# Optimization experiments

Measured on AMD Instinct MI355X. Metric: run time of the kernel, lower is better.

Reference implementation:

```python
import jax, jax.numpy as jnp
import numpy as np

WS = 8          # window_size
NH = 4          # num_heads
C = 128         # embed_dim
HD = C // NH    # head_dim
HID = 4 * C     # mlp hidden
EPS = 1e-5


def _rel_pos_index(ws):
    coords = np.stack(np.meshgrid(np.arange(ws), np.arange(ws), indexing='ij')).reshape(2, -1)
    rel = coords[:, :, None] - coords[:, None, :]          # (2, N, N)
    rel = rel.transpose(1, 2, 0).astype(np.int64)          # (N, N, 2)
    rel[..., 0] += ws - 1
    rel[..., 1] += ws - 1
    rel[..., 0] *= 2 * ws - 1
    return rel.sum(-1)                                     # (N, N)


def _layernorm(x, g, b):
    mu = jnp.mean(x, axis=-1, keepdims=True)
    var = jnp.mean(jnp.square(x - mu), axis=-1, keepdims=True)
    return (x - mu) * jax.lax.rsqrt(var + EPS) * g + b


def setup_inputs() -> dict:
    key = jax.random.key(0)
    ks = jax.random.split(key, 12)
    B, L = 32, 4096
    s = 0.02
    return {
        'x': jax.random.normal(ks[0], (B, L, C), jnp.float32),
        'W_qkv': jax.random.normal(ks[1], (C, 3 * C), jnp.float32) * s,
        'b_qkv': jnp.zeros((3 * C,), jnp.float32),
        'W_out': jax.random.normal(ks[2], (C, C), jnp.float32) * s,
        'b_out': jnp.zeros((C,), jnp.float32),
        'bias_table': jax.random.normal(ks[3], ((2 * WS - 1) ** 2, NH), jnp.float32) * s,
        'g1': jnp.ones((C,), jnp.float32), 'be1': jnp.zeros((C,), jnp.float32),
        'g2': jnp.ones((C,), jnp.float32), 'be2': jnp.zeros((C,), jnp.float32),
        'W_fc1': jax.random.normal(ks[4], (C, HID), jnp.float32) * s,
        'b_fc1': jnp.zeros((HID,), jnp.float32),
        'W_fc2': jax.random.normal(ks[5], (HID, C), jnp.float32) * s,
        'b_fc2': jnp.zeros((C,), jnp.float32),
        'H': 64, 'W': 64,
    }


def reference(x, W_qkv, b_qkv, W_out, b_out, bias_table, g1, be1, g2, be2,
              W_fc1, b_fc1, W_fc2, b_fc2, H, W):
    B, L, _ = x.shape
    N = WS * WS
    shortcut = x
    xn = _layernorm(x, g1, be1)
    # window partition: (B,H,W,C) -> (B*nw, N, C)
    xw = xn.reshape(B, H // WS, WS, W // WS, WS, C)
    xw = xw.transpose(0, 1, 3, 2, 4, 5).reshape(-1, N, C)
    # attention
    qkv = (xw @ W_qkv + b_qkv).reshape(-1, N, 3, NH, HD)
    q, k, v = jnp.moveaxis(qkv, 2, 0)                      # each (Bw, N, NH, HD)
    attn = jnp.einsum('bnhd,bmhd->bhnm', q, k) * (HD ** -0.5)
    idx = jnp.asarray(_rel_pos_index(WS))                  # (N, N)
    bias = bias_table[idx].transpose(2, 0, 1)              # (NH, N, N)
    attn = jax.nn.softmax((attn + bias[None]).astype(jnp.float32), axis=-1).astype(x.dtype)
    o = jnp.einsum('bhnm,bmhd->bnhd', attn, v).reshape(-1, N, C)
    o = o @ W_out + b_out
    # window reverse
    o = o.reshape(B, H // WS, W // WS, WS, WS, C)
    o = o.transpose(0, 1, 3, 2, 4, 5).reshape(B, L, C)
    x = shortcut + o
    # MLP block
    xn = _layernorm(x, g2, be2)
    h = jax.nn.gelu(xn @ W_fc1 + b_fc1, approximate=False)
    return x + (h @ W_fc2 + b_fc2)
```

## Files before the change

kernel.cpp:

```cpp
#include <hip/hip_runtime.h>
#include <hip/hip_bf16.h>

typedef __bf16 bf16;
typedef __bf16 bf16x8 __attribute__((ext_vector_type(8)));
typedef float f32x4 __attribute__((ext_vector_type(4)));

#define C_DIM 128
#define LDA 136
#define LDQ 40
#define LDVT 72
#define LDP 72
#define LDH 264

__device__ __forceinline__ f32x4 mfma16(bf16x8 a, bf16x8 b, f32x4 c) {
  return __builtin_amdgcn_mfma_f32_16x16x32_bf16(a, b, c, 0, 0, 0);
}


__global__ __launch_bounds__(256, 2) void swin_fused(
    const float* __restrict__ x,
    const bf16*  __restrict__ Wqkv_t, const float* __restrict__ b_qkv,
    const bf16*  __restrict__ Wout_t, const float* __restrict__ b_out,
    const float* __restrict__ btabx,
    const float* __restrict__ g1, const float* __restrict__ be1,
    const float* __restrict__ g2, const float* __restrict__ be2,
    const bf16*  __restrict__ Wfc1_t, const float* __restrict__ b_fc1,
    const bf16*  __restrict__ Wfc2_t, const float* __restrict__ b_fc2,
    float* __restrict__ out)
{
  __shared__ __attribute__((aligned(16))) char smem[76800];
  bf16 (*sA)[LDA]       = (bf16(*)[LDA])(smem);
  bf16 (*sQ)[64][LDQ]   = (bf16(*)[64][LDQ])(smem + 17408);
  bf16 (*sK)[64][LDQ]   = (bf16(*)[64][LDQ])(smem + 37888);
  bf16 (*sVT)[32][LDVT] = (bf16(*)[32][LDVT])(smem + 58368);
  bf16 (*sP)[64][LDP]   = (bf16(*)[64][LDP])(smem + 17408);
  bf16 (*sY)[LDA]       = (bf16(*)[LDA])(smem + 17408);
  bf16 (*sH)[LDH]       = (bf16(*)[LDH])(smem + 17408);

  const int tid = threadIdx.x;
  const int w   = tid >> 6;
  const int l   = tid & 63;
  const int l15 = l & 15;
  const int lhi = l >> 4;

  const int win = blockIdx.x;
  const int b   = win >> 6;
  const int wy  = (win >> 3) & 7;
  const int wx  = win & 7;
  const int rowbase = b * 4096 + wy * 512 + wx * 8;

  float yreg[2][4][4];

  {
    const int tok = tid >> 2, seg = tid & 3;
    const int t = rowbase + (tok >> 3) * 64 + (tok & 7);
    const float* xr = x + (size_t)t * C_DIM + seg * 32;
    float f[32]; float s = 0.f, s2 = 0.f;
    #pragma unroll
    for (int i = 0; i < 8; i++) {
      f32x4 v = *(const f32x4*)(xr + i * 4);
      #pragma unroll
      for (int j = 0; j < 4; j++) { float a = v[j]; f[i*4+j] = a; s += a; s2 += a*a; }
    }
    s  += __shfl_xor(s, 1);  s  += __shfl_xor(s, 2);
    s2 += __shfl_xor(s2, 1); s2 += __shfl_xor(s2, 2);
    float mu = s * (1.f/128.f);
    float rs = rsqrtf(s2 * (1.f/128.f) - mu*mu + 1e-5f);
    #pragma unroll
    for (int i = 0; i < 4; i++) {
      f32x4 gv0 = *(const f32x4*)(g1  + seg*32 + i*8);
      f32x4 gv1 = *(const f32x4*)(g1  + seg*32 + i*8 + 4);
      f32x4 bv0 = *(const f32x4*)(be1 + seg*32 + i*8);
      f32x4 bv1 = *(const f32x4*)(be1 + seg*32 + i*8 + 4);
      bf16x8 o;
      #pragma unroll
      for (int j = 0; j < 4; j++) {
        o[j]   = (bf16)((f[i*8+j]   - mu) * rs * gv0[j] + bv0[j]);
        o[j+4] = (bf16)((f[i*8+j+4] - mu) * rs * gv1[j] + bv1[j]);
      }
      *(bf16x8*)&sA[tok][seg*32 + i*8] = o;
    }
  }
  __syncthreads();

  {
    bf16x8 a[4][4];
    #pragma unroll
    for (int mt = 0; mt < 4; mt++)
      #pragma unroll
      for (int ks = 0; ks < 4; ks++)
        a[mt][ks] = *(const bf16x8*)&sA[mt*16 + l15][ks*32 + lhi*8];
    const float scale = 0.17677669529663687f;
    #pragma unroll
    for (int nti = 0; nti < 6; nti++) {
      const int nt = w * 6 + nti;
      const int colg = nt * 16 + l15;
      const bf16* wp = Wqkv_t + (size_t)colg * 128 + lhi * 8;
      bf16x8 bw[4];
      #pragma unroll
      for (int ks = 0; ks < 4; ks++) bw[ks] = *(const bf16x8*)(wp + ks * 32);
      const float bias = b_qkv[colg];
      const int kind = colg >> 7;
      const int h    = (colg >> 5) & 3;
      const int d    = colg & 31;
      #pragma unroll
      for (int mt = 0; mt < 4; mt++) {
        f32x4 acc = {0.f, 0.f, 0.f, 0.f};
        #pragma unroll
        for (int ks = 0; ks < 4; ks++) acc = mfma16(a[mt][ks], bw[ks], acc);
        #pragma unroll
        for (int r = 0; r < 4; r++) {
          const int token = mt*16 + lhi*4 + r;
          float v = acc[r] + bias;
          if (kind == 0)      sQ[h][token][d] = (bf16)(v * scale);
          else if (kind == 1) sK[h][token][d] = (bf16)v;
          else                sVT[h][d][token] = (bf16)v;
        }
      }
    }
  }
  __syncthreads();

  {
    const int h = w;
    bf16x8 aq[4], bk[4];
    #pragma unroll
    for (int mt = 0; mt < 4; mt++) aq[mt] = *(const bf16x8*)&sQ[h][mt*16 + l15][lhi*8];
    #pragma unroll
    for (int ct = 0; ct < 4; ct++) bk[ct] = *(const bf16x8*)&sK[h][ct*16 + l15][lhi*8];
    f32x4 sc[4][4];
    #pragma unroll
    for (int mt = 0; mt < 4; mt++)
      #pragma unroll
      for (int ct = 0; ct < 4; ct++) {
        f32x4 z = {0.f, 0.f, 0.f, 0.f};
        sc[mt][ct] = mfma16(aq[mt], bk[ct], z);
      }
    __syncthreads();
    #pragma unroll
    for (int mt = 0; mt < 4; mt++) {
      #pragma unroll
      for (int r = 0; r < 4; r++) {
        const int n = mt*16 + lhi*4 + r;
        f32x4 bv = *(const f32x4*)(btabx + (((h*64 + n)*16 + l15) << 2));
        float rv[4];
        #pragma unroll
        for (int ct = 0; ct < 4; ct++) rv[ct] = sc[mt][ct][r] + bv[ct];
        float mx = fmaxf(fmaxf(rv[0], rv[1]), fmaxf(rv[2], rv[3]));
        #pragma unroll
        for (int o = 1; o < 16; o <<= 1) mx = fmaxf(mx, __shfl_xor(mx, o));
        float sum = 0.f;
        #pragma unroll
        for (int ct = 0; ct < 4; ct++) { rv[ct] = __expf(rv[ct] - mx); sum += rv[ct]; }
        #pragma unroll
        for (int o = 1; o < 16; o <<= 1) sum += __shfl_xor(sum, o);
        const float inv = 1.f / sum;
        #pragma unroll
        for (int ct = 0; ct < 4; ct++) sP[h][n][ct*16 + l15] = (bf16)(rv[ct] * inv);
      }
    }
    f32x4 o_[4][2];
    #pragma unroll
    for (int mt = 0; mt < 4; mt++) { f32x4 z = {0.f,0.f,0.f,0.f}; o_[mt][0] = z; o_[mt][1] = z; }
    #pragma unroll
    for (int ks = 0; ks < 2; ks++) {
      bf16x8 ap[4], bvv[2];
      #pragma unroll
      for (int mt = 0; mt < 4; mt++) ap[mt] = *(const bf16x8*)&sP[h][mt*16 + l15][ks*32 + lhi*8];
      #pragma unroll
      for (int c2 = 0; c2 < 2; c2++) bvv[c2] = *(const bf16x8*)&sVT[h][c2*16 + l15][ks*32 + lhi*8];
      #pragma unroll
      for (int mt = 0; mt < 4; mt++)
        #pragma unroll
        for (int c2 = 0; c2 < 2; c2++) o_[mt][c2] = mfma16(ap[mt], bvv[c2], o_[mt][c2]);
    }
    #pragma unroll
    for (int mt = 0; mt < 4; mt++)
      #pragma unroll
      for (int c2 = 0; c2 < 2; c2++)
        #pragma unroll
        for (int r = 0; r < 4; r++)
          sA[mt*16 + lhi*4 + r][h*32 + c2*16 + l15] = (bf16)o_[mt][c2][r];
  }
  __syncthreads();

  {
    bf16x8 a[4][4];
    #pragma unroll
    for (int mt = 0; mt < 4; mt++)
      #pragma unroll
      for (int ks = 0; ks < 4; ks++)
        a[mt][ks] = *(const bf16x8*)&sA[mt*16 + l15][ks*32 + lhi*8];
    #pragma unroll
    for (int nto = 0; nto < 2; nto++) {
      const int col = (w*2 + nto) * 16 + l15;
      const bf16* wp = Wout_t + (size_t)col * 128 + lhi * 8;
      bf16x8 bw[4];
      #pragma unroll
      for (int ks = 0; ks < 4; ks++) bw[ks] = *(const bf16x8*)(wp + ks * 32);
      const float bo = b_out[col];
      #pragma unroll
      for (int mt = 0; mt < 4; mt++) {
        f32x4 acc = {0.f, 0.f, 0.f, 0.f};
        #pragma unroll
        for (int ks = 0; ks < 4; ks++) acc = mfma16(a[mt][ks], bw[ks], acc);
        #pragma unroll
        for (int r = 0; r < 4; r++) {
          const int token = mt*16 + lhi*4 + r;
          const int t = rowbase + (token >> 3) * 64 + (token & 7);
          float v = acc[r] + bo + x[(size_t)t * C_DIM + col];
          yreg[nto][mt][r] = v;
          sY[token][col] = (bf16)v;
        }
      }
    }
  }
  __syncthreads();

  {
    const int tok = tid >> 2, seg = tid & 3;
    float f[32]; float s = 0.f, s2 = 0.f;
    #pragma unroll
    for (int i = 0; i < 4; i++) {
      bf16x8 v = *(const bf16x8*)&sY[tok][seg*32 + i*8];
      #pragma unroll
      for (int j = 0; j < 8; j++) { float a = (float)v[j]; f[i*8+j] = a; s += a; s2 += a*a; }
    }
    s  += __shfl_xor(s, 1);  s  += __shfl_xor(s, 2);
    s2 += __shfl_xor(s2, 1); s2 += __shfl_xor(s2, 2);
    float mu = s * (1.f/128.f);
    float rs = rsqrtf(s2 * (1.f/128.f) - mu*mu + 1e-5f);
    #pragma unroll
    for (int i = 0; i < 4; i++) {
      f32x4 gv0 = *(const f32x4*)(g2  + seg*32 + i*8);
      f32x4 gv1 = *(const f32x4*)(g2  + seg*32 + i*8 + 4);
      f32x4 bv0 = *(const f32x4*)(be2 + seg*32 + i*8);
      f32x4 bv1 = *(const f32x4*)(be2 + seg*32 + i*8 + 4);
      bf16x8 o;
      #pragma unroll
      for (int j = 0; j < 4; j++) {
        o[j]   = (bf16)((f[i*8+j]   - mu) * rs * gv0[j] + bv0[j]);
        o[j+4] = (bf16)((f[i*8+j+4] - mu) * rs * gv1[j] + bv1[j]);
      }
      *(bf16x8*)&sA[tok][seg*32 + i*8] = o;
    }
  }
  __syncthreads();

  {
    bf16x8 a[4][4];
    #pragma unroll
    for (int mt = 0; mt < 4; mt++)
      #pragma unroll
      for (int ks = 0; ks < 4; ks++)
        a[mt][ks] = *(const bf16x8*)&sA[mt*16 + l15][ks*32 + lhi*8];
    f32x4 accF[2][4];
    #pragma unroll
    for (int i = 0; i < 2; i++)
      #pragma unroll
      for (int mt = 0; mt < 4; mt++) { f32x4 z = {0.f,0.f,0.f,0.f}; accF[i][mt] = z; }

    #pragma unroll
    for (int hf = 0; hf < 2; hf++) {
      #pragma unroll
      for (int nti = 0; nti < 4; nti++) {
        const int ntg    = hf*16 + w*4 + nti;
        const int colh   = ntg*16 + l15;
        const int colloc = (w*4 + nti)*16 + l15;
        const bf16* wp = Wfc1_t + (size_t)colh * 128 + lhi * 8;
        bf16x8 bw[4];
        #pragma unroll
        for (int ks = 0; ks < 4; ks++) bw[ks] = *(const bf16x8*)(wp + ks * 32);
        const float bb = b_fc1[colh];
        #pragma unroll
        for (int mt = 0; mt < 4; mt++) {
          f32x4 acc = {0.f, 0.f, 0.f, 0.f};
          #pragma unroll
          for (int ks = 0; ks < 4; ks++) acc = mfma16(a[mt][ks], bw[ks], acc);
          #pragma unroll
          for (int r = 0; r < 4; r++) {
            float v = acc[r] + bb;
            float u = v * (0.7978845608028654f + 0.0356774081363001f * v * v);
            float e = __expf(2.f * u);
            float th = 1.f - 2.f / (e + 1.f);
            float g = 0.5f * v * (1.f + th);
            sH[mt*16 + lhi*4 + r][colloc] = (bf16)g;
          }
        }
      }
      __syncthreads();
      #pragma unroll
      for (int ks = 0; ks < 8; ks++) {
        bf16x8 ah[4], bw2[2];
        #pragma unroll
        for (int mt = 0; mt < 4; mt++) ah[mt] = *(const bf16x8*)&sH[mt*16 + l15][ks*32 + lhi*8];
        #pragma unroll
        for (int nto = 0; nto < 2; nto++)
          bw2[nto] = *(const bf16x8*)(Wfc2_t + (size_t)((w*2 + nto)*16 + l15) * 512 + hf*256 + ks*32 + lhi*8);
        #pragma unroll
        for (int nto = 0; nto < 2; nto++)
          #pragma unroll
          for (int mt = 0; mt < 4; mt++) accF[nto][mt] = mfma16(ah[mt], bw2[nto], accF[nto][mt]);
      }
      __syncthreads();
    }
    #pragma unroll
    for (int nto = 0; nto < 2; nto++) {
      const int col = (w*2 + nto)*16 + l15;
      const float bb = b_fc2[col];
      #pragma unroll
      for (int mt = 0; mt < 4; mt++)
        #pragma unroll
        for (int r = 0; r < 4; r++) {
          const int token = mt*16 + lhi*4 + r;
          const int t = rowbase + (token >> 3) * 64 + (token & 7);
          out[(size_t)t * C_DIM + col] = accF[nto][mt][r] + bb + yreg[nto][mt][r];
        }
    }
  }
}

__global__ void prep_transpose(
    const float* __restrict__ Wqkv, const float* __restrict__ Wout,
    const float* __restrict__ Wfc1, const float* __restrict__ Wfc2,
    const float* __restrict__ btab,
    bf16* __restrict__ Wqkv_t, bf16* __restrict__ Wout_t,
    bf16* __restrict__ Wfc1_t, bf16* __restrict__ Wfc2_t,
    float* __restrict__ btabx)
{
  int i = blockIdx.x * 256 + threadIdx.x;
  if (i < 49152) { int n = i >> 7, k = i & 127; Wqkv_t[i] = (bf16)Wqkv[k*384 + n]; return; }
  i -= 49152;
  if (i < 16384) { int n = i >> 7, k = i & 127; Wout_t[i] = (bf16)Wout[k*128 + n]; return; }
  i -= 16384;
  if (i < 65536) { int n = i >> 7, k = i & 127; Wfc1_t[i] = (bf16)Wfc1[k*512 + n]; return; }
  i -= 65536;
  if (i < 65536) { int n = i >> 9, k = i & 511; Wfc2_t[i] = (bf16)Wfc2[k*128 + n]; return; }
  i -= 65536;
  if (i < 16384) {
    int ct  = i & 3;
    int l15 = (i >> 2) & 15;
    int n   = (i >> 6) & 63;
    int h   = i >> 12;
    int m = ct * 16 + l15;
    int nr = n >> 3, nc = n & 7, mr = m >> 3, mc = m & 7;
    int idx = (nr - mr + 7) * 15 + (nc - mc + 7);
    btabx[i] = btab[idx * 4 + h];
  }
}

extern "C" void kernel_launch(void* const* d_in, const int* in_sizes, int n_in,
                              void* d_out, int out_size, void* d_ws, size_t ws_size,
                              hipStream_t stream)
{
  const float* x    = (const float*)d_in[0];
  const float* Wqkv = (const float*)d_in[1];
  const float* bqkv = (const float*)d_in[2];
  const float* Wout = (const float*)d_in[3];
  const float* bout = (const float*)d_in[4];
  const float* btab = (const float*)d_in[5];
  const float* g1   = (const float*)d_in[6];
  const float* be1  = (const float*)d_in[7];
  const float* g2   = (const float*)d_in[8];
  const float* be2  = (const float*)d_in[9];
  const float* Wfc1 = (const float*)d_in[10];
  const float* bfc1 = (const float*)d_in[11];
  const float* Wfc2 = (const float*)d_in[12];
  const float* bfc2 = (const float*)d_in[13];

  bf16* ws = (bf16*)d_ws;
  bf16* Wqkv_t = ws;
  bf16* Wout_t = ws + 49152;
  bf16* Wfc1_t = ws + 65536;
  bf16* Wfc2_t = ws + 131072;
  float* btabx = (float*)(ws + 196608);

  prep_transpose<<<832, 256, 0, stream>>>(Wqkv, Wout, Wfc1, Wfc2, btab,
                                          Wqkv_t, Wout_t, Wfc1_t, Wfc2_t, btabx);

  const int B = in_sizes[0] / (4096 * 128);
  swin_fused<<<dim3(B * 64), 256, 0, stream>>>(
      x, Wqkv_t, bqkv, Wout_t, bout, btabx, g1, be1, g2, be2,
      Wfc1_t, bfc1, Wfc2_t, bfc2, (float*)d_out);
}
```

Before: 195.0 us.

## Double block to 512 threads and halve per-wave work across all stages

Launches 8 waves per window instead of 4. Each stage is split more finely: LayerNorm uses 8 lanes per token, QKV uses 3 tiles per wave, attention gives each head's 64 query rows to two waves, and the out-proj/FC1/FC2 stages use one 16-column tile per wave. The fp32 residual registers are dropped; the residual is kept as bf16 in shared memory (sY moved to the sVT region) and re-read for the final add, which lowers residual precision. The new launch bounds of (512,4) cap registers much more tightly, so spills are possible, and LDS use of about 75KB per block still limits how many blocks fit on a CU.

```diff
diff --git a/kernel.cpp b/kernel.cpp
--- a/kernel.cpp
+++ b/kernel.cpp
@@ -17,7 +17,7 @@
 }
 
 
-__global__ __launch_bounds__(256, 2) void swin_fused(
+__global__ __launch_bounds__(512, 4) void swin_fused(
     const float* __restrict__ x,
     const bf16*  __restrict__ Wqkv_t, const float* __restrict__ b_qkv,
     const bf16*  __restrict__ Wout_t, const float* __restrict__ b_out,
@@ -32,10 +32,10 @@
   bf16 (*sA)[LDA]       = (bf16(*)[LDA])(smem);
   bf16 (*sQ)[64][LDQ]   = (bf16(*)[64][LDQ])(smem + 17408);
   bf16 (*sK)[64][LDQ]   = (bf16(*)[64][LDQ])(smem + 37888);
+  bf16 (*sP)[64][LDP]   = (bf16(*)[64][LDP])(smem + 17408);
+  bf16 (*sH)[LDH]       = (bf16(*)[LDH])(smem + 17408);
   bf16 (*sVT)[32][LDVT] = (bf16(*)[32][LDVT])(smem + 58368);
-  bf16 (*sP)[64][LDP]   = (bf16(*)[64][LDP])(smem + 17408);
-  bf16 (*sY)[LDA]       = (bf16(*)[LDA])(smem + 17408);
-  bf16 (*sH)[LDH]       = (bf16(*)[LDH])(smem + 17408);
+  bf16 (*sY)[LDA]       = (bf16(*)[LDA])(smem + 58368);
 
   const int tid = threadIdx.x;
   const int w   = tid >> 6;
@@ -49,36 +49,34 @@
   const int wx  = win & 7;
   const int rowbase = b * 4096 + wy * 512 + wx * 8;
 
-  float yreg[2][4][4];
-
-  {
-    const int tok = tid >> 2, seg = tid & 3;
+  {
+    const int tok = tid >> 3, seg = tid & 7;
     const int t = rowbase + (tok >> 3) * 64 + (tok & 7);
-    const float* xr = x + (size_t)t * C_DIM + seg * 32;
-    float f[32]; float s = 0.f, s2 = 0.f;
-    #pragma unroll
-    for (int i = 0; i < 8; i++) {
+    const float* xr = x + (size_t)t * C_DIM + seg * 16;
+    float f[16]; float s = 0.f, s2 = 0.f;
+    #pragma unroll
+    for (int i = 0; i < 4; i++) {
       f32x4 v = *(const f32x4*)(xr + i * 4);
       #pragma unroll
       for (int j = 0; j < 4; j++) { float a = v[j]; f[i*4+j] = a; s += a; s2 += a*a; }
     }
-    s  += __shfl_xor(s, 1);  s  += __shfl_xor(s, 2);
-    s2 += __shfl_xor(s2, 1); s2 += __shfl_xor(s2, 2);
+    s  += __shfl_xor(s, 1);  s  += __shfl_xor(s, 2);  s  += __shfl_xor(s, 4);
+    s2 += __shfl_xor(s2, 1); s2 += __shfl_xor(s2, 2); s2 += __shfl_xor(s2, 4);
     float mu = s * (1.f/128.f);
     float rs = rsqrtf(s2 * (1.f/128.f) - mu*mu + 1e-5f);
     #pragma unroll
-    for (int i = 0; i < 4; i++) {
-      f32x4 gv0 = *(const f32x4*)(g1  + seg*32 + i*8);
-      f32x4 gv1 = *(const f32x4*)(g1  + seg*32 + i*8 + 4);
-      f32x4 bv0 = *(const f32x4*)(be1 + seg*32 + i*8);
-      f32x4 bv1 = *(const f32x4*)(be1 + seg*32 + i*8 + 4);
+    for (int i = 0; i < 2; i++) {
+      f32x4 gv0 = *(const f32x4*)(g1  + seg*16 + i*8);
+      f32x4 gv1 = *(const f32x4*)(g1  + seg*16 + i*8 + 4);
+      f32x4 bv0 = *(const f32x4*)(be1 + seg*16 + i*8);
+      f32x4 bv1 = *(const f32x4*)(be1 + seg*16 + i*8 + 4);
       bf16x8 o;
       #pragma unroll
       for (int j = 0; j < 4; j++) {
         o[j]   = (bf16)((f[i*8+j]   - mu) * rs * gv0[j] + bv0[j]);
         o[j+4] = (bf16)((f[i*8+j+4] - mu) * rs * gv1[j] + bv1[j]);
       }
-      *(bf16x8*)&sA[tok][seg*32 + i*8] = o;
+      *(bf16x8*)&sA[tok][seg*16 + i*8] = o;
     }
   }
   __syncthreads();
@@ -92,8 +90,8 @@
         a[mt][ks] = *(const bf16x8*)&sA[mt*16 + l15][ks*32 + lhi*8];
     const float scale = 0.17677669529663687f;
     #pragma unroll
-    for (int nti = 0; nti < 6; nti++) {
-      const int nt = w * 6 + nti;
+    for (int nti = 0; nti < 3; nti++) {
+      const int nt = w * 3 + nti;
       const int colg = nt * 16 + l15;
       const bf16* wp = Wqkv_t + (size_t)colg * 128 + lhi * 8;
       bf16x8 bw[4];
@@ -122,30 +120,32 @@
   __syncthreads();
 
   {
-    const int h = w;
-    bf16x8 aq[4], bk[4];
-    #pragma unroll
-    for (int mt = 0; mt < 4; mt++) aq[mt] = *(const bf16x8*)&sQ[h][mt*16 + l15][lhi*8];
+    const int h    = w >> 1;
+    const int half = w & 1;
+    bf16x8 aq[2], bk[4];
+    #pragma unroll
+    for (int mtl = 0; mtl < 2; mtl++)
+      aq[mtl] = *(const bf16x8*)&sQ[h][(half*2 + mtl)*16 + l15][lhi*8];
     #pragma unroll
     for (int ct = 0; ct < 4; ct++) bk[ct] = *(const bf16x8*)&sK[h][ct*16 + l15][lhi*8];
-    f32x4 sc[4][4];
-    #pragma unroll
-    for (int mt = 0; mt < 4; mt++)
+    f32x4 sc[2][4];
+    #pragma unroll
+    for (int mtl = 0; mtl < 2; mtl++)
       #pragma unroll
       for (int ct = 0; ct < 4; ct++) {
         f32x4 z = {0.f, 0.f, 0.f, 0.f};
-        sc[mt][ct] = mfma16(aq[mt], bk[ct], z);
+        sc[mtl][ct] = mfma16(aq[mtl], bk[ct], z);
       }
     __syncthreads();
     #pragma unroll
-    for (int mt = 0; mt < 4; mt++) {
+    for (int mtl = 0; mtl < 2; mtl++) {
       #pragma unroll
       for (int r = 0; r < 4; r++) {
-        const int n = mt*16 + lhi*4 + r;
+        const int n = (half*2 + mtl)*16 + lhi*4 + r;
         f32x4 bv = *(const f32x4*)(btabx + (((h*64 + n)*16 + l15) << 2));
         float rv[4];
         #pragma unroll
-        for (int ct = 0; ct < 4; ct++) rv[ct] = sc[mt][ct][r] + bv[ct];
+        for (int ct = 0; ct < 4; ct++) rv[ct] = sc[mtl][ct][r] + bv[ct];
         float mx = fmaxf(fmaxf(rv[0], rv[1]), fmaxf(rv[2], rv[3]));
         #pragma unroll
         for (int o = 1; o < 16; o <<= 1) mx = fmaxf(mx, __shfl_xor(mx, o));
@@ -159,28 +159,30 @@
         for (int ct = 0; ct < 4; ct++) sP[h][n][ct*16 + l15] = (bf16)(rv[ct] * inv);
       }
     }
-    f32x4 o_[4][2];
-    #pragma unroll
-    for (int mt = 0; mt < 4; mt++) { f32x4 z = {0.f,0.f,0.f,0.f}; o_[mt][0] = z; o_[mt][1] = z; }
+    f32x4 o_[2][2];
+    #pragma unroll
+    for (int mtl = 0; mtl < 2; mtl++) { f32x4 z = {0.f,0.f,0.f,0.f}; o_[mtl][0] = z; o_[mtl][1] = z; }
     #pragma unroll
     for (int ks = 0; ks < 2; ks++) {
-      bf16x8 ap[4], bvv[2];
-      #pragma unroll
-      for (int mt = 0; mt < 4; mt++) ap[mt] = *(const bf16x8*)&sP[h][mt*16 + l15][ks*32 + lhi*8];
-      #pragma unroll
-      for (int c2 = 0; c2 < 2; c2++) bvv[c2] = *(const bf16x8*)&sVT[h][c2*16 + l15][ks*32 + lhi*8];
-      #pragma unroll
-      for (int mt = 0; mt < 4; mt++)
-        #pragma unroll
-        for (int c2 = 0; c2 < 2; c2++) o_[mt][c2] = mfma16(ap[mt], bvv[c2], o_[mt][c2]);
-    }
-    #pragma unroll
-    for (int mt = 0; mt < 4; mt++)
+      bf16x8 ap[2], bvv[2];
+      #pragma unroll
+      for (int mtl = 0; mtl < 2; mtl++)
+        ap[mtl] = *(const bf16x8*)&sP[h][(half*2 + mtl)*16 + l15][ks*32 + lhi*8];
       #pragma unroll
       for (int c2 = 0; c2 < 2; c2++)
+        bvv[c2] = *(const bf16x8*)&sVT[h][c2*16 + l15][ks*32 + lhi*8];
+      #pragma unroll
+      for (int mtl = 0; mtl < 2; mtl++)
+        #pragma unroll
+        for (int c2 = 0; c2 < 2; c2++) o_[mtl][c2] = mfma16(ap[mtl], bvv[c2], o_[mtl][c2]);
+    }
+    #pragma unroll
+    for (int mtl = 0; mtl < 2; mtl++)
+      #pragma unroll
+      for (int c2 = 0; c2 < 2; c2++)
         #pragma unroll
         for (int r = 0; r < 4; r++)
-          sA[mt*16 + lhi*4 + r][h*32 + c2*16 + l15] = (bf16)o_[mt][c2][r];
+          sA[(half*2 + mtl)*16 + lhi*4 + r][h*32 + c2*16 + l15] = (bf16)o_[mtl][c2][r];
   }
   __syncthreads();
 
@@ -191,58 +193,54 @@
       #pragma unroll
       for (int ks = 0; ks < 4; ks++)
         a[mt][ks] = *(const bf16x8*)&sA[mt*16 + l15][ks*32 + lhi*8];
-    #pragma unroll
-    for (int nto = 0; nto < 2; nto++) {
-      const int col = (w*2 + nto) * 16 + l15;
-      const bf16* wp = Wout_t + (size_t)col * 128 + lhi * 8;
-      bf16x8 bw[4];
-      #pragma unroll
-      for (int ks = 0; ks < 4; ks++) bw[ks] = *(const bf16x8*)(wp + ks * 32);
-      const float bo = b_out[col];
-      #pragma unroll
-      for (int mt = 0; mt < 4; mt++) {
-        f32x4 acc = {0.f, 0.f, 0.f, 0.f};
-        #pragma unroll
-        for (int ks = 0; ks < 4; ks++) acc = mfma16(a[mt][ks], bw[ks], acc);
-        #pragma unroll
-        for (int r = 0; r < 4; r++) {
-          const int token = mt*16 + lhi*4 + r;
-          const int t = rowbase + (token >> 3) * 64 + (token & 7);
-          float v = acc[r] + bo + x[(size_t)t * C_DIM + col];
-          yreg[nto][mt][r] = v;
-          sY[token][col] = (bf16)v;
-        }
-      }
-    }
-  }
-  __syncthreads();
-
-  {
-    const int tok = tid >> 2, seg = tid & 3;
-    float f[32]; float s = 0.f, s2 = 0.f;
-    #pragma unroll
-    for (int i = 0; i < 4; i++) {
-      bf16x8 v = *(const bf16x8*)&sY[tok][seg*32 + i*8];
+    const int col = w * 16 + l15;
+    const bf16* wp = Wout_t + (size_t)col * 128 + lhi * 8;
+    bf16x8 bw[4];
+    #pragma unroll
+    for (int ks = 0; ks < 4; ks++) bw[ks] = *(const bf16x8*)(wp + ks * 32);
+    const float bo = b_out[col];
+    #pragma unroll
+    for (int mt = 0; mt < 4; mt++) {
+      f32x4 acc = {0.f, 0.f, 0.f, 0.f};
+      #pragma unroll
+      for (int ks = 0; ks < 4; ks++) acc = mfma16(a[mt][ks], bw[ks], acc);
+      #pragma unroll
+      for (int r = 0; r < 4; r++) {
+        const int token = mt*16 + lhi*4 + r;
+        const int t = rowbase + (token >> 3) * 64 + (token & 7);
+        float v = acc[r] + bo + x[(size_t)t * C_DIM + col];
+        sY[token][col] = (bf16)v;
+      }
+    }
+  }
+  __syncthreads();
+
+  {
+    const int tok = tid >> 3, seg = tid & 7;
+    float f[16]; float s = 0.f, s2 = 0.f;
+    #pragma unroll
+    for (int i = 0; i < 2; i++) {
+      bf16x8 v = *(const bf16x8*)&sY[tok][seg*16 + i*8];
       #pragma unroll
       for (int j = 0; j < 8; j++) { float a = (float)v[j]; f[i*8+j] = a; s += a; s2 += a*a; }
     }
-    s  += __shfl_xor(s, 1);  s  += __shfl_xor(s, 2);
-    s2 += __shfl_xor(s2, 1); s2 += __shfl_xor(s2, 2);
+    s  += __shfl_xor(s, 1);  s  += __shfl_xor(s, 2);  s  += __shfl_xor(s, 4);
+    s2 += __shfl_xor(s2, 1); s2 += __shfl_xor(s2, 2); s2 += __shfl_xor(s2, 4);
     float mu = s * (1.f/128.f);
     float rs = rsqrtf(s2 * (1.f/128.f) - mu*mu + 1e-5f);
     #pragma unroll
-    for (int i = 0; i < 4; i++) {
-      f32x4 gv0 = *(const f32x4*)(g2  + seg*32 + i*8);
-      f32x4 gv1 = *(const f32x4*)(g2  + seg*32 + i*8 + 4);
-      f32x4 bv0 = *(const f32x4*)(be2 + seg*32 + i*8);
-      f32x4 bv1 = *(const f32x4*)(be2 + seg*32 + i*8 + 4);
+    for (int i = 0; i < 2; i++) {
+      f32x4 gv0 = *(const f32x4*)(g2  + seg*16 + i*8);
+      f32x4 gv1 = *(const f32x4*)(g2  + seg*16 + i*8 + 4);
+      f32x4 bv0 = *(const f32x4*)(be2 + seg*16 + i*8);
+      f32x4 bv1 = *(const f32x4*)(be2 + seg*16 + i*8 + 4);
       bf16x8 o;
       #pragma unroll
       for (int j = 0; j < 4; j++) {
         o[j]   = (bf16)((f[i*8+j]   - mu) * rs * gv0[j] + bv0[j]);
         o[j+4] = (bf16)((f[i*8+j+4] - mu) * rs * gv1[j] + bv1[j]);
       }
-      *(bf16x8*)&sA[tok][seg*32 + i*8] = o;
+      *(bf16x8*)&sA[tok][seg*16 + i*8] = o;
     }
   }
   __syncthreads();
@@ -254,19 +252,17 @@
       #pragma unroll
       for (int ks = 0; ks < 4; ks++)
         a[mt][ks] = *(const bf16x8*)&sA[mt*16 + l15][ks*32 + lhi*8];
-    f32x4 accF[2][4];
-    #pragma unroll
-    for (int i = 0; i < 2; i++)
-      #pragma unroll
-      for (int mt = 0; mt < 4; mt++) { f32x4 z = {0.f,0.f,0.f,0.f}; accF[i][mt] = z; }
+    f32x4 accF[4];
+    #pragma unroll
+    for (int mt = 0; mt < 4; mt++) { f32x4 z = {0.f,0.f,0.f,0.f}; accF[mt] = z; }
 
     #pragma unroll
     for (int hf = 0; hf < 2; hf++) {
       #pragma unroll
-      for (int nti = 0; nti < 4; nti++) {
-        const int ntg    = hf*16 + w*4 + nti;
+      for (int nti = 0; nti < 2; nti++) {
+        const int ntg    = hf*16 + w*2 + nti;
         const int colh   = ntg*16 + l15;
-        const int colloc = (w*4 + nti)*16 + l15;
+        const int colloc = (w*2 + nti)*16 + l15;
         const bf16* wp = Wfc1_t + (size_t)colh * 128 + lhi * 8;
         bf16x8 bw[4];
         #pragma unroll
@@ -291,32 +287,25 @@
       __syncthreads();
       #pragma unroll
       for (int ks = 0; ks < 8; ks++) {
-        bf16x8 ah[4], bw2[2];
+        bf16x8 ah[4];
         #pragma unroll
         for (int mt = 0; mt < 4; mt++) ah[mt] = *(const bf16x8*)&sH[mt*16 + l15][ks*32 + lhi*8];
-        #pragma unroll
-        for (int nto = 0; nto < 2; nto++)
-          bw2[nto] = *(const bf16x8*)(Wfc2_t + (size_t)((w*2 + nto)*16 + l15) * 512 + hf*256 + ks*32 + lhi*8);
-        #pragma unroll
-        for (int nto = 0; nto < 2; nto++)
-          #pragma unroll
-          for (int mt = 0; mt < 4; mt++) accF[nto][mt] = mfma16(ah[mt], bw2[nto], accF[nto][mt]);
+        bf16x8 bw2 = *(const bf16x8*)(Wfc2_t + (size_t)(w*16 + l15) * 512 + hf*256 + ks*32 + lhi*8);
+        #pragma unroll
+        for (int mt = 0; mt < 4; mt++) accF[mt] = mfma16(ah[mt], bw2, accF[mt]);
       }
       __syncthreads();
     }
-    #pragma unroll
-    for (int nto = 0; nto < 2; nto++) {
-      const int col = (w*2 + nto)*16 + l15;
-      const float bb = b_fc2[col];
-      #pragma unroll
-      for (int mt = 0; mt < 4; mt++)
-        #pragma unroll
-        for (int r = 0; r < 4; r++) {
-          const int token = mt*16 + lhi*4 + r;
-          const int t = rowbase + (token >> 3) * 64 + (token & 7);
-          out[(size_t)t * C_DIM + col] = accF[nto][mt][r] + bb + yreg[nto][mt][r];
-        }
-    }
+    const int col = w*16 + l15;
+    const float bb = b_fc2[col];
+    #pragma unroll
+    for (int mt = 0; mt < 4; mt++)
+      #pragma unroll
+      for (int r = 0; r < 4; r++) {
+        const int token = mt*16 + lhi*4 + r;
+        const int t = rowbase + (token >> 3) * 64 + (token & 7);
+        out[(size_t)t * C_DIM + col] = accF[mt][r] + bb + (float)sY[token][col];
+      }
   }
 }
 
@@ -379,7 +368,7 @@
                                           Wqkv_t, Wout_t, Wfc1_t, Wfc2_t, btabx);
 
   const int B = in_sizes[0] / (4096 * 128);
-  swin_fused<<<dim3(B * 64), 256, 0, stream>>>(
+  swin_fused<<<dim3(B * 64), 512, 0, stream>>>(
       x, Wqkv_t, bqkv, Wout_t, bout, btabx, g1, be1, g2, be2,
       Wfc1_t, bfc1, Wfc2_t, bfc2, (float*)d_out);
 }
```

New measurement: 194.6 us. No clear change (-0.2%).

## Software-prefetch weight tiles and residual inputs into registers ahead of MFMA use

Applied to the files above, without the earlier changes.

Adds register double-buffering for the global weight loads in the QKV, output-projection, FC1 and FC2 GEMMs. Each next weight tile is issued before the current MFMAs run, and the W_out weights and residual x values are loaded during the softmax phase. The goal is to hide global memory latency behind compute in each stage. It raises register pressure under launch_bounds(256,2), which could cause spills or lower occupancy.

```diff
diff --git a/kernel.cpp b/kernel.cpp
--- a/kernel.cpp
+++ b/kernel.cpp
@@ -91,15 +91,25 @@
       for (int ks = 0; ks < 4; ks++)
         a[mt][ks] = *(const bf16x8*)&sA[mt*16 + l15][ks*32 + lhi*8];
     const float scale = 0.17677669529663687f;
+    bf16x8 bw[4]; float bias;
+    {
+      const int colg0 = (w*6)*16 + l15;
+      const bf16* wp = Wqkv_t + (size_t)colg0 * 128 + lhi * 8;
+      #pragma unroll
+      for (int ks = 0; ks < 4; ks++) bw[ks] = *(const bf16x8*)(wp + ks * 32);
+      bias = b_qkv[colg0];
+    }
     #pragma unroll
     for (int nti = 0; nti < 6; nti++) {
-      const int nt = w * 6 + nti;
-      const int colg = nt * 16 + l15;
-      const bf16* wp = Wqkv_t + (size_t)colg * 128 + lhi * 8;
-      bf16x8 bw[4];
-      #pragma unroll
-      for (int ks = 0; ks < 4; ks++) bw[ks] = *(const bf16x8*)(wp + ks * 32);
-      const float bias = b_qkv[colg];
+      const int colg = (w*6 + nti) * 16 + l15;
+      bf16x8 bwn[4]; float biasn = 0.f;
+      if (nti < 5) {
+        const int colgn = (w*6 + nti + 1) * 16 + l15;
+        const bf16* wpn = Wqkv_t + (size_t)colgn * 128 + lhi * 8;
+        #pragma unroll
+        for (int ks = 0; ks < 4; ks++) bwn[ks] = *(const bf16x8*)(wpn + ks * 32);
+        biasn = b_qkv[colgn];
+      }
       const int kind = colg >> 7;
       const int h    = (colg >> 5) & 3;
       const int d    = colg & 31;
@@ -117,9 +127,18 @@
           else                sVT[h][d][token] = (bf16)v;
         }
       }
+      if (nti < 5) {
+        #pragma unroll
+        for (int ks = 0; ks < 4; ks++) bw[ks] = bwn[ks];
+        bias = biasn;
+      }
     }
   }
   __syncthreads();
+
+  bf16x8 pwO[2][4];
+  float  px[2][4][4];
+  float  pbO[2];
 
   {
     const int h = w;
@@ -137,6 +156,22 @@
         sc[mt][ct] = mfma16(aq[mt], bk[ct], z);
       }
     __syncthreads();
+    #pragma unroll
+    for (int nto = 0; nto < 2; nto++) {
+      const int col = (w*2 + nto) * 16 + l15;
+      const bf16* wp = Wout_t + (size_t)col * 128 + lhi * 8;
+      #pragma unroll
+      for (int ks = 0; ks < 4; ks++) pwO[nto][ks] = *(const bf16x8*)(wp + ks * 32);
+      pbO[nto] = b_out[col];
+      #pragma unroll
+      for (int mt = 0; mt < 4; mt++)
+        #pragma unroll
+        for (int r = 0; r < 4; r++) {
+          const int token = mt*16 + lhi*4 + r;
+          const int t = rowbase + (token >> 3) * 64 + (token & 7);
+          px[nto][mt][r] = x[(size_t)t * C_DIM + col];
+        }
+    }
     #pragma unroll
     for (int mt = 0; mt < 4; mt++) {
       #pragma unroll
@@ -194,21 +229,15 @@
     #pragma unroll
     for (int nto = 0; nto < 2; nto++) {
       const int col = (w*2 + nto) * 16 + l15;
-      const bf16* wp = Wout_t + (size_t)col * 128 + lhi * 8;
-      bf16x8 bw[4];
-      #pragma unroll
-      for (int ks = 0; ks < 4; ks++) bw[ks] = *(const bf16x8*)(wp + ks * 32);
-      const float bo = b_out[col];
       #pragma unroll
       for (int mt = 0; mt < 4; mt++) {
         f32x4 acc = {0.f, 0.f, 0.f, 0.f};
         #pragma unroll
-        for (int ks = 0; ks < 4; ks++) acc = mfma16(a[mt][ks], bw[ks], acc);
+        for (int ks = 0; ks < 4; ks++) acc = mfma16(a[mt][ks], pwO[nto][ks], acc);
         #pragma unroll
         for (int r = 0; r < 4; r++) {
           const int token = mt*16 + lhi*4 + r;
-          const int t = rowbase + (token >> 3) * 64 + (token & 7);
-          float v = acc[r] + bo + x[(size_t)t * C_DIM + col];
+          float v = acc[r] + pbO[nto] + px[nto][mt][r];
           yreg[nto][mt][r] = v;
           sY[token][col] = (bf16)v;
         }
@@ -217,7 +246,18 @@
   }
   __syncthreads();
 
-  {
+  bf16x8 pw1[4][4];
+  float  pb1[4];
+
+  {
+    #pragma unroll
+    for (int nti = 0; nti < 4; nti++) {
+      const int colh = (w*4 + nti) * 16 + l15;
+      const bf16* wp = Wfc1_t + (size_t)colh * 128 + lhi * 8;
+      #pragma unroll
+      for (int ks = 0; ks < 4; ks++) pw1[nti][ks] = *(const bf16x8*)(wp + ks * 32);
+      pb1[nti] = b_fc1[colh];
+    }
     const int tok = tid >> 2, seg = tid & 3;
     float f[32]; float s = 0.f, s2 = 0.f;
     #pragma unroll
@@ -264,14 +304,18 @@
     for (int hf = 0; hf < 2; hf++) {
       #pragma unroll
       for (int nti = 0; nti < 4; nti++) {
-        const int ntg    = hf*16 + w*4 + nti;
-        const int colh   = ntg*16 + l15;
+        bf16x8 bw[4];
+        #pragma unroll
+        for (int ks = 0; ks < 4; ks++) bw[ks] = pw1[nti][ks];
+        const float bb = pb1[nti];
+        if (hf == 0) {
+          const int colh1 = (16 + w*4 + nti) * 16 + l15;
+          const bf16* wp1 = Wfc1_t + (size_t)colh1 * 128 + lhi * 8;
+          #pragma unroll
+          for (int ks = 0; ks < 4; ks++) pw1[nti][ks] = *(const bf16x8*)(wp1 + ks * 32);
+          pb1[nti] = b_fc1[colh1];
+        }
         const int colloc = (w*4 + nti)*16 + l15;
-        const bf16* wp = Wfc1_t + (size_t)colh * 128 + lhi * 8;
-        bf16x8 bw[4];
-        #pragma unroll
-        for (int ks = 0; ks < 4; ks++) bw[ks] = *(const bf16x8*)(wp + ks * 32);
-        const float bb = b_fc1[colh];
         #pragma unroll
         for (int mt = 0; mt < 4; mt++) {
           f32x4 acc = {0.f, 0.f, 0.f, 0.f};
@@ -289,18 +333,25 @@
         }
       }
       __syncthreads();
+      bf16x8 bw2[2];
+      #pragma unroll
+      for (int nto = 0; nto < 2; nto++)
+        bw2[nto] = *(const bf16x8*)(Wfc2_t + (size_t)((w*2 + nto)*16 + l15) * 512 + hf*256 + lhi*8);
       #pragma unroll
       for (int ks = 0; ks < 8; ks++) {
-        bf16x8 ah[4], bw2[2];
+        bf16x8 ah[4], bw2n[2];
+        if (ks < 7) {
+          #pragma unroll
+          for (int nto = 0; nto < 2; nto++)
+            bw2n[nto] = *(const bf16x8*)(Wfc2_t + (size_t)((w*2 + nto)*16 + l15) * 512 + hf*256 + (ks+1)*32 + lhi*8);
+        }
         #pragma unroll
         for (int mt = 0; mt < 4; mt++) ah[mt] = *(const bf16x8*)&sH[mt*16 + l15][ks*32 + lhi*8];
-        #pragma unroll
-        for (int nto = 0; nto < 2; nto++)
-          bw2[nto] = *(const bf16x8*)(Wfc2_t + (size_t)((w*2 + nto)*16 + l15) * 512 + hf*256 + ks*32 + lhi*8);
         #pragma unroll
         for (int nto = 0; nto < 2; nto++)
           #pragma unroll
           for (int mt = 0; mt < 4; mt++) accF[nto][mt] = mfma16(ah[mt], bw2[nto], accF[nto][mt]);
+        if (ks < 7) { bw2[0] = bw2n[0]; bw2[1] = bw2n[1]; }
       }
       __syncthreads();
     }
```

After: 232.1 us. +19.0%, slower.
